# Performance work log

Measured on AMD Instinct MI355X. Metric: run time of the kernel, lower is better.

Reference implementation:

```python
import jax, jax.numpy as jnp
import numpy as np

N_NODES = 50000
N_EDGES = 800000
HIDDEN = 128
HEADS = 4
LAYERS = 2
NEG_SLOPE = 0.2


def setup_inputs() -> dict:
    key = jax.random.key(0)
    ks = jax.random.split(key, 12)
    s_in = 1.0 / np.sqrt(HIDDEN)
    x = jax.random.normal(ks[0], (N_NODES, HIDDEN), dtype=jnp.float32)
    edge_index = jax.random.randint(ks[1], (2, N_EDGES), 0, N_NODES, dtype=jnp.int64)
    conv_w = jax.random.normal(ks[2], (LAYERS, HIDDEN, HEADS * HIDDEN), dtype=jnp.float32) * s_in
    att_src = jax.random.normal(ks[3], (LAYERS, HEADS, HIDDEN), dtype=jnp.float32) * s_in
    att_dst = jax.random.normal(ks[4], (LAYERS, HEADS, HIDDEN), dtype=jnp.float32) * s_in
    conv_b = jax.random.normal(ks[5], (LAYERS, HIDDEN), dtype=jnp.float32) * 0.01
    proj_w = jax.random.normal(ks[6], (LAYERS, HIDDEN, HIDDEN), dtype=jnp.float32) * s_in
    proj_b = jax.random.normal(ks[7], (LAYERS, HIDDEN), dtype=jnp.float32) * 0.01
    skip_w = jax.random.normal(ks[8], (LAYERS, HIDDEN, HIDDEN), dtype=jnp.float32) * s_in
    skip_b = jax.random.normal(ks[9], (LAYERS, HIDDEN), dtype=jnp.float32) * 0.01
    return {"x": x, "edge_index": edge_index, "conv_w": conv_w, "att_src": att_src,
            "att_dst": att_dst, "conv_b": conv_b, "proj_w": proj_w, "proj_b": proj_b,
            "skip_w": skip_w, "skip_b": skip_b}


def _gat_layer(x, src, dst, W, a_s, a_d, b):
    # x: [N, D]; W: [D, H*C]; a_s, a_d: [H, C]; b: [C]
    N = x.shape[0]
    h = (x @ W).reshape(N, HEADS, HIDDEN)          # [N, H, C]
    alpha_src = jnp.einsum('nhc,hc->nh', h, a_s)   # [N, H]
    alpha_dst = jnp.einsum('nhc,hc->nh', h, a_d)   # [N, H]
    alpha = alpha_src[src] + alpha_dst[dst]        # [E, H]
    alpha = jnp.where(alpha >= 0, alpha, NEG_SLOPE * alpha)  # leaky_relu(0.2)
    amax = jax.ops.segment_max(alpha, dst, num_segments=N)   # [N, H]
    ex = jnp.exp(alpha - amax[dst])                # [E, H]
    denom = jax.ops.segment_sum(ex, dst, num_segments=N)     # [N, H]
    w = ex / (denom[dst] + 1e-16)                  # PyG softmax eps
    msg = h[src] * w[:, :, None]                   # [E, H, C]
    out = jax.ops.segment_sum(msg, dst, num_segments=N)      # [N, H, C]
    return out.mean(axis=1) + b                    # concat=False -> head mean


def reference(x, edge_index, conv_w, att_src, att_dst, conv_b, proj_w, proj_b, skip_w, skip_b):
    src, dst = edge_index[0], edge_index[1]
    out = x
    for l in range(LAYERS):
        conv = _gat_layer(out, src, dst, conv_w[l], att_src[l], att_dst[l], conv_b[l])
        out = jax.nn.relu(conv) @ proj_w[l] + proj_b[l] + (out @ skip_w[l] + skip_b[l])
    return out
```

## Files before the change

### kernel.cpp

```cpp
#include <hip/hip_runtime.h>
#include <hip/hip_bf16.h>
#include <stdint.h>

#define N_NODES 50000
#define N_EDGES 800000
#define HIDDEN  128
#define HEADS   4
#define HD      (HEADS*HIDDEN)
#define CAST_Q  (N_NODES*HIDDEN/4)

typedef __attribute__((ext_vector_type(8))) short  short8;
typedef __attribute__((ext_vector_type(4))) float  floatx4;
typedef __attribute__((ext_vector_type(2))) float  floatx2;

static __device__ __forceinline__ unsigned short bf16_bits(float f) {
    __hip_bfloat16 h = __float2bfloat16(f);
    union { __hip_bfloat16 b; unsigned short s; } u; u.b = h; return u.s;
}

static __device__ __forceinline__ float lexp(float a) {
    return __expf(fmaxf(a, 0.2f * a));
}


#if __has_builtin(__builtin_amdgcn_cvt_pk_fp8_f32) && __has_builtin(__builtin_amdgcn_cvt_pk_f32_fp8)
#define FP8_HW 1
#else
#define FP8_HW 0
static __device__ __forceinline__ unsigned fp8_enc1(float f) {
    unsigned s = __float_as_uint(f) >> 31;
    float a = fabsf(f);
    if (a < 0.0009765625f) return s << 7;
    if (a > 448.f) a = 448.f;
    unsigned ub = __float_as_uint(a) + 0x00080000u;
    int e = (int)((ub >> 23) & 255) - 120;
    unsigned m = (ub >> 20) & 7;
    if (e <= 0) {
        int mm = (int)(a * 512.f + 0.5f); if (mm > 7) mm = 7;
        return (s << 7) | (unsigned)mm;
    }
    if (e > 15) { e = 15; m = 7; }
    return (s << 7) | ((unsigned)e << 3) | m;
}
static __device__ __forceinline__ float fp8_dec1(unsigned b) {
    unsigned s = (b >> 7) & 1, e = (b >> 3) & 15, m = b & 7;
    if (e == 0) { float f = (float)m * 0.001953125f; return s ? -f : f; }
    return __uint_as_float((s << 31) | ((e + 120) << 23) | (m << 20));
}
#endif

static __device__ __forceinline__ unsigned fp8_pack4(float a, float b, float c, float d) {
#if FP8_HW
    int w = __builtin_amdgcn_cvt_pk_fp8_f32(a, b, 0, false);
    w     = __builtin_amdgcn_cvt_pk_fp8_f32(c, d, w, true);
    return (unsigned)w;
#else
    return fp8_enc1(a) | (fp8_enc1(b) << 8) | (fp8_enc1(c) << 16) | (fp8_enc1(d) << 24);
#endif
}

static __device__ __forceinline__ void accf8(float* acc, uint2 u, float wt) {
#if FP8_HW
    floatx2 f;
    f = __builtin_amdgcn_cvt_pk_f32_fp8((int)u.x, false); acc[0] += wt * f.x; acc[1] += wt * f.y;
    f = __builtin_amdgcn_cvt_pk_f32_fp8((int)u.x, true);  acc[2] += wt * f.x; acc[3] += wt * f.y;
    f = __builtin_amdgcn_cvt_pk_f32_fp8((int)u.y, false); acc[4] += wt * f.x; acc[5] += wt * f.y;
    f = __builtin_amdgcn_cvt_pk_f32_fp8((int)u.y, true);  acc[6] += wt * f.x; acc[7] += wt * f.y;
#else
    acc[0] += wt * fp8_dec1(u.x & 255);         acc[1] += wt * fp8_dec1((u.x >> 8) & 255);
    acc[2] += wt * fp8_dec1((u.x >> 16) & 255); acc[3] += wt * fp8_dec1(u.x >> 24);
    acc[4] += wt * fp8_dec1(u.y & 255);         acc[5] += wt * fp8_dec1((u.y >> 8) & 255);
    acc[6] += wt * fp8_dec1((u.y >> 16) & 255); acc[7] += wt * fp8_dec1(u.y >> 24);
#endif
}


__global__ __launch_bounds__(256) void prep_k(
        const float* __restrict__ x, unsigned short* __restrict__ xb16,
        const float* __restrict__ conv_w, const float* __restrict__ proj_w,
        const float* __restrict__ skip_w,
        unsigned short* __restrict__ cwb, unsigned short* __restrict__ pwb,
        unsigned short* __restrict__ swb) {
    int i = blockIdx.x * 256 + threadIdx.x;
    if (i < CAST_Q) {
        float4 v = ((const float4*)x)[i];
        uint2 p;
        p.x = (unsigned)bf16_bits(v.x) | ((unsigned)bf16_bits(v.y) << 16);
        p.y = (unsigned)bf16_bits(v.z) | ((unsigned)bf16_bits(v.w) << 16);
        ((uint2*)xb16)[i] = p;
        return;
    }
    int o = i - CAST_Q;
    const float* B; unsigned short* D; int off, N; bool perm = false;
    if (o < 131072)      { B = conv_w + (o >> 16) * 65536; D = cwb + (o >> 16) * 65536; off = o & 65535; N = 512; }
    else if (o < 163840) { int t = o - 131072; B = proj_w + (t >> 14) * 16384; D = pwb + (t >> 14) * 16384; off = t & 16383; N = 128; perm = true; }
    else if (o < 196608) { int t = o - 163840; B = skip_w + (t >> 14) * 16384; D = swb + (t >> 14) * 16384; off = t & 16383; N = 128; }
    else return;
    int j = off & 7, r = (off >> 3) & 15, q = (off >> 7) & 3;
    int rest = off >> 9, ntn = N >> 4;
    int nt = rest % ntn, kc = rest / ntn;
    int kr = kc * 32 + q * 8 + j;
    int row = perm ? ((kr & 7) * 16 + (kr >> 3)) : kr;
    D[off] = bf16_bits(B[(size_t)row * N + nt * 16 + r]);
}


__global__ __launch_bounds__(256) void hist_k(const int* __restrict__ dst,
                                              int* __restrict__ cnt, int E) {
    int e = blockIdx.x * 256 + threadIdx.x;
    if (e < E) atomicAdd(&cnt[dst[e]], 1);
}

__global__ __launch_bounds__(1024) void scan1_k(const int* __restrict__ cnt,
                                                int* __restrict__ row_ptr,
                                                int* __restrict__ bsum, int n) {
    __shared__ int buf[1024];
    int t = threadIdx.x, i = blockIdx.x * 1024 + t;
    int v = (i < n) ? cnt[i] : 0;
    buf[t] = v;
    __syncthreads();
    for (int off = 1; off < 1024; off <<= 1) {
        int xv = (t >= off) ? buf[t - off] : 0;
        __syncthreads();
        buf[t] += xv;
        __syncthreads();
    }
    if (i < n) row_ptr[i] = buf[t] - v;
    if (t == 1023) bsum[blockIdx.x] = buf[1023];
}

__global__ void scan2_k(int* __restrict__ bsum, int nb) {
    if (threadIdx.x == 0) {
        int acc = 0;
        for (int i = 0; i < nb; ++i) { int v = bsum[i]; bsum[i] = acc; acc += v; }
    }
}

__global__ __launch_bounds__(1024) void scan3_k(int* __restrict__ row_ptr,
                                                const int* __restrict__ bsum, int n, int E) {
    int i = blockIdx.x * 1024 + threadIdx.x;
    if (i < n) row_ptr[i] += bsum[blockIdx.x];
    if (i == 0) row_ptr[n] = E;
}

__global__ __launch_bounds__(256) void scatter_k(const int* __restrict__ src,
                                                 const int* __restrict__ dst,
                                                 const int* __restrict__ row_ptr,
                                                 int* __restrict__ fill,
                                                 int* __restrict__ src_sorted, int E) {
    int e = blockIdx.x * 256 + threadIdx.x;
    if (e >= E) return;
    int d = dst[e];
    int p = row_ptr[d] + atomicAdd(&fill[d], 1);
    src_sorted[p] = src[e];
}


__global__ __launch_bounds__(256, 2) void gemmc_k(
        const __hip_bfloat16* __restrict__ A,
        const unsigned short* __restrict__ Bs,
        const float* __restrict__ att_s, const float* __restrict__ att_d,
        unsigned char* __restrict__ h8,
        float* __restrict__ a_src, float* __restrict__ a_dst, int mtiles) {
    int head = threadIdx.x >> 6;
    int lane = threadIdx.x & 63;
    int r = lane & 15, q = lane >> 4;

    short8 Bf[4][8];
#pragma unroll
    for (int kc = 0; kc < 4; ++kc)
#pragma unroll
        for (int ntl = 0; ntl < 8; ++ntl)
            Bf[kc][ntl] = *(const short8*)((const short*)Bs +
                (((size_t)(kc * 32 + head * 8 + ntl) * 4 + q) * 128 + r * 8));

    float as_r[8], ad_r[8];
#pragma unroll
    for (int ntl = 0; ntl < 8; ++ntl) {
        as_r[ntl] = att_s[head * HIDDEN + ntl * 16 + r];
        ad_r[ntl] = att_d[head * HIDDEN + ntl * 16 + r];
    }

    for (int mt = blockIdx.x; mt < mtiles; mt += gridDim.x) {
        int m0 = mt * 16;
        const short* Ab = (const short*)A + (size_t)(m0 + r) * HIDDEN + q * 8;
        short8 av[4];
#pragma unroll
        for (int kc = 0; kc < 4; ++kc) av[kc] = *(const short8*)(Ab + kc * 32);

        floatx4 acc[8];
#pragma unroll
        for (int i = 0; i < 8; ++i) acc[i] = (floatx4){0.f, 0.f, 0.f, 0.f};
#pragma unroll
        for (int kc = 0; kc < 4; ++kc)
#pragma unroll
            for (int ntl = 0; ntl < 8; ++ntl)
                acc[ntl] = __builtin_amdgcn_mfma_f32_16x16x32_bf16(av[kc], Bf[kc][ntl], acc[ntl], 0, 0, 0);

#pragma unroll
        for (int i = 0; i < 4; ++i) {
            uint2 o;
            o.x = fp8_pack4(acc[0][i], acc[1][i], acc[2][i], acc[3][i]);
            o.y = fp8_pack4(acc[4][i], acc[5][i], acc[6][i], acc[7][i]);
            *(uint2*)(h8 + (size_t)(m0 + q * 4 + i) * HD + head * HIDDEN + r * 8) = o;
        }
        float sA[4] = {0, 0, 0, 0}, sD[4] = {0, 0, 0, 0};
#pragma unroll
        for (int ntl = 0; ntl < 8; ++ntl)
#pragma unroll
            for (int i = 0; i < 4; ++i) {
                sA[i] += acc[ntl][i] * as_r[ntl];
                sD[i] += acc[ntl][i] * ad_r[ntl];
            }
#pragma unroll
        for (int d = 1; d < 16; d <<= 1)
#pragma unroll
            for (int i = 0; i < 4; ++i) {
                sA[i] += __shfl_xor(sA[i], d);
                sD[i] += __shfl_xor(sD[i], d);
            }
        if (r == 0)
#pragma unroll
            for (int i = 0; i < 4; ++i) {
                int row = m0 + q * 4 + i;
                a_src[row * HEADS + head] = sA[i];
                a_dst[row * HEADS + head] = sD[i];
            }
    }
}


template <typename OutT>
__global__ __launch_bounds__(256, 2) void gemmp_k(
        const __hip_bfloat16* __restrict__ A,  const unsigned short* __restrict__ Bs,
        const __hip_bfloat16* __restrict__ A2, const unsigned short* __restrict__ Bs2,
        const float* __restrict__ b1, const float* __restrict__ b2,
        OutT* __restrict__ D, int mtiles) {
    int wave = threadIdx.x >> 6;
    int lane = threadIdx.x & 63;
    int r = lane & 15, q = lane >> 4;
    int nh = wave & 1;

    short8 Bf[4][4], Bf2[4][4];
#pragma unroll
    for (int kc = 0; kc < 4; ++kc)
#pragma unroll
        for (int ntl = 0; ntl < 4; ++ntl) {
            size_t off = (((size_t)(kc * 8 + nh * 4 + ntl) * 4 + q) * 128 + r * 8);
            Bf[kc][ntl]  = *(const short8*)((const short*)Bs  + off);
            Bf2[kc][ntl] = *(const short8*)((const short*)Bs2 + off);
        }
    float bias[4];
#pragma unroll
    for (int ntl = 0; ntl < 4; ++ntl) {
        int col = nh * 64 + ntl * 16 + r;
        bias[ntl] = b1[col] + b2[col];
    }

    for (int mt = blockIdx.x * 2 + (wave >> 1); mt < mtiles; mt += gridDim.x * 2) {
        int m0 = mt * 16;
        const short* Ab  = (const short*)A  + (size_t)(m0 + r) * HIDDEN + q * 8;
        const short* Ab2 = (const short*)A2 + (size_t)(m0 + r) * HIDDEN + q * 8;
        short8 av[4], av2[4];
#pragma unroll
        for (int kc = 0; kc < 4; ++kc) {
            av[kc]  = *(const short8*)(Ab  + kc * 32);
            av2[kc] = *(const short8*)(Ab2 + kc * 32);
        }
        floatx4 acc[4];
#pragma unroll
        for (int i = 0; i < 4; ++i) acc[i] = (floatx4){0.f, 0.f, 0.f, 0.f};
#pragma unroll
        for (int kc = 0; kc < 4; ++kc)
#pragma unroll
            for (int ntl = 0; ntl < 4; ++ntl) {
                acc[ntl] = __builtin_amdgcn_mfma_f32_16x16x32_bf16(av[kc],  Bf[kc][ntl],  acc[ntl], 0, 0, 0);
                acc[ntl] = __builtin_amdgcn_mfma_f32_16x16x32_bf16(av2[kc], Bf2[kc][ntl], acc[ntl], 0, 0, 0);
            }
#pragma unroll
        for (int ntl = 0; ntl < 4; ++ntl) {
            int col = nh * 64 + ntl * 16 + r;
#pragma unroll
            for (int i = 0; i < 4; ++i) {
                int row = m0 + q * 4 + i;
                float v = acc[ntl][i] + bias[ntl];
                if constexpr (sizeof(OutT) == 4)
                    ((float*)D)[(size_t)row * HIDDEN + col] = v;
                else
                    ((__hip_bfloat16*)D)[(size_t)row * HIDDEN + col] = __float2bfloat16(v);
            }
        }
    }
}


__global__ __launch_bounds__(256) void msg_k(const int* __restrict__ row_ptr,
                                             const int* __restrict__ src_sorted,
                                             const float* __restrict__ a_src,
                                             const float* __restrict__ a_dst,
                                             const unsigned char* __restrict__ h8,
                                             const float* __restrict__ conv_b,
                                             __hip_bfloat16* __restrict__ rc) {
    int wave = threadIdx.x >> 6;
    int lane = threadIdx.x & 63;
    int n = blockIdx.x * 4 + wave;
    if (n >= N_NODES) return;
    int head = lane >> 4;
    float adn = a_dst[n * HEADS + head];
    int beg = row_ptr[n], end = row_ptr[n + 1];
    const uint2* hq = (const uint2*)h8;

    float acc[8] = {0.f, 0.f, 0.f, 0.f, 0.f, 0.f, 0.f, 0.f};
    float esum = 0.f;
    for (int base = beg; base < end; base += 32) {
        int m = min(32, end - base);
        int sv = (lane < m) ? src_sorted[base + lane] : 0;
        int j = 0;
        for (; j + 4 <= m; j += 4) {
            int s0 = __shfl(sv, j),     s1 = __shfl(sv, j + 1);
            int s2 = __shfl(sv, j + 2), s3 = __shfl(sv, j + 3);
            uint2 u0 = hq[(size_t)s0 * 64 + lane];
            uint2 u1 = hq[(size_t)s1 * 64 + lane];
            uint2 u2 = hq[(size_t)s2 * 64 + lane];
            uint2 u3 = hq[(size_t)s3 * 64 + lane];
            float e0 = lexp(a_src[s0 * 4 + head] + adn);
            float e1 = lexp(a_src[s1 * 4 + head] + adn);
            float e2 = lexp(a_src[s2 * 4 + head] + adn);
            float e3 = lexp(a_src[s3 * 4 + head] + adn);
            accf8(acc, u0, e0);
            accf8(acc, u1, e1);
            accf8(acc, u2, e2);
            accf8(acc, u3, e3);
            esum += (e0 + e1) + (e2 + e3);
        }
        for (; j < m; ++j) {
            int s0 = __shfl(sv, j);
            uint2 u0 = hq[(size_t)s0 * 64 + lane];
            float e0 = lexp(a_src[s0 * 4 + head] + adn);
            accf8(acc, u0, e0);
            esum += e0;
        }
    }
    float rinv = 1.f / (esum + 1e-16f);
#pragma unroll
    for (int k = 0; k < 8; ++k) acc[k] *= rinv;
#pragma unroll
    for (int k = 0; k < 8; ++k) {
        acc[k] += __shfl_xor(acc[k], 16);
        acc[k] += __shfl_xor(acc[k], 32);
    }
    if (lane < 16) {
        union { uint4 v; unsigned short us[8]; } o;
#pragma unroll
        for (int k = 0; k < 8; ++k) {
            float mres = 0.25f * acc[k] + conv_b[k * 16 + lane];
            o.us[k] = bf16_bits(mres > 0.f ? mres : 0.f);
        }
        ((uint4*)rc)[(size_t)n * 16 + lane] = o.v;
    }
}


extern "C" void kernel_launch(void* const* d_in, const int* in_sizes, int n_in,
                              void* d_out, int out_size, void* d_ws, size_t ws_size,
                              hipStream_t stream) {
    const float* x      = (const float*)d_in[0];
    const int*   ei     = (const int*)d_in[1];
    const float* conv_w = (const float*)d_in[2];
    const float* att_s  = (const float*)d_in[3];
    const float* att_d  = (const float*)d_in[4];
    const float* conv_b = (const float*)d_in[5];
    const float* proj_w = (const float*)d_in[6];
    const float* proj_b = (const float*)d_in[7];
    const float* skip_w = (const float*)d_in[8];
    const float* skip_b = (const float*)d_in[9];
    float* out = (float*)d_out;

    char* ws = (char*)d_ws;
    size_t o = 0;
    auto alloc = [&](size_t b) { size_t c = o; o += (b + 255) & ~(size_t)255; return c; };
    __hip_bfloat16* xb16 = (__hip_bfloat16*)(ws + alloc((size_t)N_NODES * HIDDEN * 2));
    unsigned short* cwb  = (unsigned short*)(ws + alloc((size_t)2 * HIDDEN * HD * 2));
    unsigned short* pwb  = (unsigned short*)(ws + alloc((size_t)2 * HIDDEN * HIDDEN * 2));
    unsigned short* swb  = (unsigned short*)(ws + alloc((size_t)2 * HIDDEN * HIDDEN * 2));
    unsigned char* h8    = (unsigned char*)(ws + alloc((size_t)N_NODES * HD));
    float* a_src         = (float*)(ws + alloc((size_t)N_NODES * HEADS * 4));
    float* a_dst         = (float*)(ws + alloc((size_t)N_NODES * HEADS * 4));
    int* row_ptr         = (int*)(ws + alloc((size_t)(N_NODES + 1) * 4));
    int* cntfill         = (int*)(ws + alloc((size_t)2 * N_NODES * 4));
    int* cnt  = cntfill;
    int* fill = cntfill + N_NODES;
    int* src_s           = (int*)(ws + alloc((size_t)N_EDGES * 4));
    __hip_bfloat16* rc   = (__hip_bfloat16*)(ws + alloc((size_t)N_NODES * HIDDEN * 2));
    __hip_bfloat16* xb   = (__hip_bfloat16*)(ws + alloc((size_t)N_NODES * HIDDEN * 2));
    int* bsum            = (int*)(ws + alloc(64 * 4));

    const int* srcp = ei;
    const int* dstp = ei + N_EDGES;

    (void)hipMemsetAsync(cntfill, 0, (size_t)2 * N_NODES * 4, stream);

    prep_k<<<(CAST_Q + 196608 + 255) / 256, 256, 0, stream>>>(
        x, (unsigned short*)xb16, conv_w, proj_w, skip_w, cwb, pwb, swb);

    hist_k<<<(N_EDGES + 255) / 256, 256, 0, stream>>>(dstp, cnt, N_EDGES);
    const int nb = (N_NODES + 1023) / 1024;
    scan1_k<<<nb, 1024, 0, stream>>>(cnt, row_ptr, bsum, N_NODES);
    scan2_k<<<1, 64, 0, stream>>>(bsum, nb);
    scan3_k<<<nb, 1024, 0, stream>>>(row_ptr, bsum, N_NODES, N_EDGES);
    scatter_k<<<(N_EDGES + 255) / 256, 256, 0, stream>>>(srcp, dstp, row_ptr, fill, src_s, N_EDGES);

    const int mtiles = N_NODES / 16;
    const __hip_bfloat16* xc = xb16;
    for (int l = 0; l < 2; ++l) {
        gemmc_k<<<512, 256, 0, stream>>>(
            xc, cwb + (size_t)l * HIDDEN * HD,
            att_s + l * HD, att_d + l * HD, h8, a_src, a_dst, mtiles);
        msg_k<<<(N_NODES + 3) / 4, 256, 0, stream>>>(
            row_ptr, src_s, a_src, a_dst, h8, conv_b + l * HIDDEN, rc);
        if (l == 0)
            gemmp_k<__hip_bfloat16><<<512, 256, 0, stream>>>(
                rc, pwb + (size_t)l * HIDDEN * HIDDEN,
                xc, swb + (size_t)l * HIDDEN * HIDDEN,
                proj_b + l * HIDDEN, skip_b + l * HIDDEN, xb, mtiles);
        else
            gemmp_k<float><<<512, 256, 0, stream>>>(
                rc, pwb + (size_t)l * HIDDEN * HIDDEN,
                xc, swb + (size_t)l * HIDDEN * HIDDEN,
                proj_b + l * HIDDEN, skip_b + l * HIDDEN, out, mtiles);
        xc = xb;
    }
}
```

Before: 359.9 us.

## Fuse message aggregation with projection and skip GEMM into one kernel

The separate message-passing kernel and the projection+skip GEMM are merged into one kernel. Each block aggregates attention-weighted neighbour features for 16 nodes, four per wave, and stages the bf16 ReLU result in LDS. It then runs the MFMA projection and skip GEMM for that 16-row tile straight from LDS. This removes the intermediate rc buffer round-trip through global memory and one launch per layer. In exchange, every block reloads the projection and skip weights from global/L2 instead of keeping them resident in registers, and the MFMA stage cannot start until all four waves finish their uneven edge loops.

```diff
diff --git a/kernel.cpp b/kernel.cpp
--- a/kernel.cpp
+++ b/kernel.cpp
@@ -8,6 +8,7 @@
 #define HEADS   4
 #define HD      (HEADS*HIDDEN)
 #define CAST_Q  (N_NODES*HIDDEN/4)
+#define NTILES  (N_NODES/16)
 
 typedef __attribute__((ext_vector_type(8))) short  short8;
 typedef __attribute__((ext_vector_type(4))) float  floatx4;
@@ -231,132 +232,109 @@
 
 
 template <typename OutT>
-__global__ __launch_bounds__(256, 2) void gemmp_k(
-        const __hip_bfloat16* __restrict__ A,  const unsigned short* __restrict__ Bs,
-        const __hip_bfloat16* __restrict__ A2, const unsigned short* __restrict__ Bs2,
+__global__ __launch_bounds__(256) void mp_k(
+        const int* __restrict__ row_ptr, const int* __restrict__ src_sorted,
+        const float* __restrict__ a_src, const float* __restrict__ a_dst,
+        const unsigned char* __restrict__ h8, const float* __restrict__ conv_b,
+        const unsigned short* __restrict__ Bs,
+        const __hip_bfloat16* __restrict__ A2,
+        const unsigned short* __restrict__ Bs2,
         const float* __restrict__ b1, const float* __restrict__ b2,
-        OutT* __restrict__ D, int mtiles) {
+        OutT* __restrict__ D) {
+    __shared__ uint4 lds[16 * 17];
     int wave = threadIdx.x >> 6;
     int lane = threadIdx.x & 63;
+    int head = lane >> 4;
     int r = lane & 15, q = lane >> 4;
-    int nh = wave & 1;
-
-    short8 Bf[4][4], Bf2[4][4];
-#pragma unroll
-    for (int kc = 0; kc < 4; ++kc)
-#pragma unroll
-        for (int ntl = 0; ntl < 4; ++ntl) {
-            size_t off = (((size_t)(kc * 8 + nh * 4 + ntl) * 4 + q) * 128 + r * 8);
-            Bf[kc][ntl]  = *(const short8*)((const short*)Bs  + off);
-            Bf2[kc][ntl] = *(const short8*)((const short*)Bs2 + off);
-        }
-    float bias[4];
-#pragma unroll
-    for (int ntl = 0; ntl < 4; ++ntl) {
-        int col = nh * 64 + ntl * 16 + r;
-        bias[ntl] = b1[col] + b2[col];
-    }
-
-    for (int mt = blockIdx.x * 2 + (wave >> 1); mt < mtiles; mt += gridDim.x * 2) {
-        int m0 = mt * 16;
-        const short* Ab  = (const short*)A  + (size_t)(m0 + r) * HIDDEN + q * 8;
-        const short* Ab2 = (const short*)A2 + (size_t)(m0 + r) * HIDDEN + q * 8;
-        short8 av[4], av2[4];
+    int m0 = blockIdx.x * 16;
+    const uint2* hq = (const uint2*)h8;
+
+    for (int i = 0; i < 4; ++i) {
+        int li = wave * 4 + i;
+        int n = m0 + li;
+        float adn = a_dst[n * HEADS + head];
+        int beg = row_ptr[n], end = row_ptr[n + 1];
+
+        float acc[8] = {0.f, 0.f, 0.f, 0.f, 0.f, 0.f, 0.f, 0.f};
+        float esum = 0.f;
+        for (int base = beg; base < end; base += 32) {
+            int m = min(32, end - base);
+            int sv = (lane < m) ? src_sorted[base + lane] : 0;
+            int j = 0;
+            for (; j + 4 <= m; j += 4) {
+                int s0 = __shfl(sv, j),     s1 = __shfl(sv, j + 1);
+                int s2 = __shfl(sv, j + 2), s3 = __shfl(sv, j + 3);
+                uint2 u0 = hq[(size_t)s0 * 64 + lane];
+                uint2 u1 = hq[(size_t)s1 * 64 + lane];
+                uint2 u2 = hq[(size_t)s2 * 64 + lane];
+                uint2 u3 = hq[(size_t)s3 * 64 + lane];
+                float e0 = lexp(a_src[s0 * 4 + head] + adn);
+                float e1 = lexp(a_src[s1 * 4 + head] + adn);
+                float e2 = lexp(a_src[s2 * 4 + head] + adn);
+                float e3 = lexp(a_src[s3 * 4 + head] + adn);
+                accf8(acc, u0, e0);
+                accf8(acc, u1, e1);
+                accf8(acc, u2, e2);
+                accf8(acc, u3, e3);
+                esum += (e0 + e1) + (e2 + e3);
+            }
+            for (; j < m; ++j) {
+                int s0 = __shfl(sv, j);
+                uint2 u0 = hq[(size_t)s0 * 64 + lane];
+                float e0 = lexp(a_src[s0 * 4 + head] + adn);
+                accf8(acc, u0, e0);
+                esum += e0;
+            }
+        }
+        float rinv = 1.f / (esum + 1e-16f);
+#pragma unroll
+        for (int k = 0; k < 8; ++k) acc[k] *= rinv;
+#pragma unroll
+        for (int k = 0; k < 8; ++k) {
+            acc[k] += __shfl_xor(acc[k], 16);
+            acc[k] += __shfl_xor(acc[k], 32);
+        }
+        if (lane < 16) {
+            union { uint4 v; unsigned short us[8]; } o;
+#pragma unroll
+            for (int k = 0; k < 8; ++k) {
+                float mres = 0.25f * acc[k] + conv_b[k * 16 + lane];
+                o.us[k] = bf16_bits(mres > 0.f ? mres : 0.f);
+            }
+            lds[li * 17 + lane] = o.v;
+        }
+    }
+    __syncthreads();
+
+    short8 av[4], av2[4];
+#pragma unroll
+    for (int kc = 0; kc < 4; ++kc) {
+        av[kc] = *(const short8*)&lds[r * 17 + kc * 4 + q];
+        av2[kc] = *(const short8*)((const short*)A2 + (size_t)(m0 + r) * HIDDEN + q * 8 + kc * 32);
+    }
+#pragma unroll
+    for (int c = 0; c < 2; ++c) {
+        int ct = wave * 2 + c;
+        floatx4 acc = (floatx4){0.f, 0.f, 0.f, 0.f};
 #pragma unroll
         for (int kc = 0; kc < 4; ++kc) {
-            av[kc]  = *(const short8*)(Ab  + kc * 32);
-            av2[kc] = *(const short8*)(Ab2 + kc * 32);
-        }
-        floatx4 acc[4];
-#pragma unroll
-        for (int i = 0; i < 4; ++i) acc[i] = (floatx4){0.f, 0.f, 0.f, 0.f};
-#pragma unroll
-        for (int kc = 0; kc < 4; ++kc)
-#pragma unroll
-            for (int ntl = 0; ntl < 4; ++ntl) {
-                acc[ntl] = __builtin_amdgcn_mfma_f32_16x16x32_bf16(av[kc],  Bf[kc][ntl],  acc[ntl], 0, 0, 0);
-                acc[ntl] = __builtin_amdgcn_mfma_f32_16x16x32_bf16(av2[kc], Bf2[kc][ntl], acc[ntl], 0, 0, 0);
-            }
-#pragma unroll
-        for (int ntl = 0; ntl < 4; ++ntl) {
-            int col = nh * 64 + ntl * 16 + r;
-#pragma unroll
-            for (int i = 0; i < 4; ++i) {
-                int row = m0 + q * 4 + i;
-                float v = acc[ntl][i] + bias[ntl];
-                if constexpr (sizeof(OutT) == 4)
-                    ((float*)D)[(size_t)row * HIDDEN + col] = v;
-                else
-                    ((__hip_bfloat16*)D)[(size_t)row * HIDDEN + col] = __float2bfloat16(v);
-            }
-        }
-    }
-}
-
-
-__global__ __launch_bounds__(256) void msg_k(const int* __restrict__ row_ptr,
-                                             const int* __restrict__ src_sorted,
-                                             const float* __restrict__ a_src,
-                                             const float* __restrict__ a_dst,
-                                             const unsigned char* __restrict__ h8,
-                                             const float* __restrict__ conv_b,
-                                             __hip_bfloat16* __restrict__ rc) {
-    int wave = threadIdx.x >> 6;
-    int lane = threadIdx.x & 63;
-    int n = blockIdx.x * 4 + wave;
-    if (n >= N_NODES) return;
-    int head = lane >> 4;
-    float adn = a_dst[n * HEADS + head];
-    int beg = row_ptr[n], end = row_ptr[n + 1];
-    const uint2* hq = (const uint2*)h8;
-
-    float acc[8] = {0.f, 0.f, 0.f, 0.f, 0.f, 0.f, 0.f, 0.f};
-    float esum = 0.f;
-    for (int base = beg; base < end; base += 32) {
-        int m = min(32, end - base);
-        int sv = (lane < m) ? src_sorted[base + lane] : 0;
-        int j = 0;
-        for (; j + 4 <= m; j += 4) {
-            int s0 = __shfl(sv, j),     s1 = __shfl(sv, j + 1);
-            int s2 = __shfl(sv, j + 2), s3 = __shfl(sv, j + 3);
-            uint2 u0 = hq[(size_t)s0 * 64 + lane];
-            uint2 u1 = hq[(size_t)s1 * 64 + lane];
-            uint2 u2 = hq[(size_t)s2 * 64 + lane];
-            uint2 u3 = hq[(size_t)s3 * 64 + lane];
-            float e0 = lexp(a_src[s0 * 4 + head] + adn);
-            float e1 = lexp(a_src[s1 * 4 + head] + adn);
-            float e2 = lexp(a_src[s2 * 4 + head] + adn);
-            float e3 = lexp(a_src[s3 * 4 + head] + adn);
-            accf8(acc, u0, e0);
-            accf8(acc, u1, e1);
-            accf8(acc, u2, e2);
-            accf8(acc, u3, e3);
-            esum += (e0 + e1) + (e2 + e3);
-        }
-        for (; j < m; ++j) {
-            int s0 = __shfl(sv, j);
-            uint2 u0 = hq[(size_t)s0 * 64 + lane];
-            float e0 = lexp(a_src[s0 * 4 + head] + adn);
-            accf8(acc, u0, e0);
-            esum += e0;
-        }
-    }
-    float rinv = 1.f / (esum + 1e-16f);
-#pragma unroll
-    for (int k = 0; k < 8; ++k) acc[k] *= rinv;
-#pragma unroll
-    for (int k = 0; k < 8; ++k) {
-        acc[k] += __shfl_xor(acc[k], 16);
-        acc[k] += __shfl_xor(acc[k], 32);
-    }
-    if (lane < 16) {
-        union { uint4 v; unsigned short us[8]; } o;
-#pragma unroll
-        for (int k = 0; k < 8; ++k) {
-            float mres = 0.25f * acc[k] + conv_b[k * 16 + lane];
-            o.us[k] = bf16_bits(mres > 0.f ? mres : 0.f);
-        }
-        ((uint4*)rc)[(size_t)n * 16 + lane] = o.v;
+            size_t off = (((size_t)(kc * 8 + ct) * 4 + q) * 128 + r * 8);
+            short8 bv  = *(const short8*)((const short*)Bs  + off);
+            short8 bv2 = *(const short8*)((const short*)Bs2 + off);
+            acc = __builtin_amdgcn_mfma_f32_16x16x32_bf16(av[kc],  bv,  acc, 0, 0, 0);
+            acc = __builtin_amdgcn_mfma_f32_16x16x32_bf16(av2[kc], bv2, acc, 0, 0, 0);
+        }
+        int col = ct * 16 + r;
+        float bias = b1[col] + b2[col];
+#pragma unroll
+        for (int i = 0; i < 4; ++i) {
+            int row = m0 + q * 4 + i;
+            float v = acc[i] + bias;
+            if constexpr (sizeof(OutT) == 4)
+                ((float*)D)[(size_t)row * HIDDEN + col] = v;
+            else
+                ((__hip_bfloat16*)D)[(size_t)row * HIDDEN + col] = __float2bfloat16(v);
+        }
     }
 }
 
@@ -391,7 +369,6 @@
     int* cnt  = cntfill;
     int* fill = cntfill + N_NODES;
     int* src_s           = (int*)(ws + alloc((size_t)N_EDGES * 4));
-    __hip_bfloat16* rc   = (__hip_bfloat16*)(ws + alloc((size_t)N_NODES * HIDDEN * 2));
     __hip_bfloat16* xb   = (__hip_bfloat16*)(ws + alloc((size_t)N_NODES * HIDDEN * 2));
     int* bsum            = (int*)(ws + alloc(64 * 4));
 
@@ -410,24 +387,21 @@
     scan3_k<<<nb, 1024, 0, stream>>>(row_ptr, bsum, N_NODES, N_EDGES);
     scatter_k<<<(N_EDGES + 255) / 256, 256, 0, stream>>>(srcp, dstp, row_ptr, fill, src_s, N_EDGES);
 
-    const int mtiles = N_NODES / 16;
     const __hip_bfloat16* xc = xb16;
     for (int l = 0; l < 2; ++l) {
         gemmc_k<<<512, 256, 0, stream>>>(
             xc, cwb + (size_t)l * HIDDEN * HD,
-            att_s + l * HD, att_d + l * HD, h8, a_src, a_dst, mtiles);
-        msg_k<<<(N_NODES + 3) / 4, 256, 0, stream>>>(
-            row_ptr, src_s, a_src, a_dst, h8, conv_b + l * HIDDEN, rc);
+            att_s + l * HD, att_d + l * HD, h8, a_src, a_dst, NTILES);
         if (l == 0)
-            gemmp_k<__hip_bfloat16><<<512, 256, 0, stream>>>(
-                rc, pwb + (size_t)l * HIDDEN * HIDDEN,
-                xc, swb + (size_t)l * HIDDEN * HIDDEN,
-                proj_b + l * HIDDEN, skip_b + l * HIDDEN, xb, mtiles);
+            mp_k<__hip_bfloat16><<<NTILES, 256, 0, stream>>>(
+                row_ptr, src_s, a_src, a_dst, h8, conv_b + l * HIDDEN,
+                pwb + (size_t)l * HIDDEN * HIDDEN, xc, swb + (size_t)l * HIDDEN * HIDDEN,
+                proj_b + l * HIDDEN, skip_b + l * HIDDEN, xb);
         else
-            gemmp_k<float><<<512, 256, 0, stream>>>(
-                rc, pwb + (size_t)l * HIDDEN * HIDDEN,
-                xc, swb + (size_t)l * HIDDEN * HIDDEN,
-                proj_b + l * HIDDEN, skip_b + l * HIDDEN, out, mtiles);
+            mp_k<float><<<NTILES, 256, 0, stream>>>(
+                row_ptr, src_s, a_src, a_dst, h8, conv_b + l * HIDDEN,
+                pwb + (size_t)l * HIDDEN * HIDDEN, xc, swb + (size_t)l * HIDDEN * HIDDEN,
+                proj_b + l * HIDDEN, skip_b + l * HIDDEN, out);
         xc = xb;
     }
 }
```

After: 386.3 us. 7.3% more time.
